# Kernel tuning notes

Hardware: AMD Instinct MI355X
Metric: run time of the kernel (lower is better)

## Reference

```python
import jax, jax.numpy as jnp
import numpy as np

N, P, T, D = 25000, 100000, 4, 128
DIN = 4 * D + 4  # 516
LEAKY = 0.001


def setup_inputs() -> dict:
    key = jax.random.key(0)
    ks = jax.random.split(key, 12)
    inp = {
        "coords": jax.random.normal(ks[0], (N, T, 3), jnp.float32),
        "propers": jax.random.randint(ks[1], (P, 4), 0, N, jnp.int64),
        "encoded": jax.random.normal(ks[2], (N, D), jnp.float32),
        "t": jax.random.uniform(ks[3], (T,), jnp.float32),
        "answer": jax.random.normal(ks[4], (N, T, 3), jnp.float32),
        # AggregateMLP(516 -> 128 -> 128 -> 128 -> 2), LeakyReLU(0.001) between
        "W0": jax.random.normal(ks[5], (DIN, D), jnp.float32) / np.sqrt(DIN),
        "b0": jnp.zeros((D,), jnp.float32),
        "W1": jax.random.normal(ks[6], (D, D), jnp.float32) / np.sqrt(D),
        "b1": jnp.zeros((D,), jnp.float32),
        "W2": jax.random.normal(ks[7], (D, D), jnp.float32) / np.sqrt(D),
        "b2": jnp.zeros((D,), jnp.float32),
        "W3": jax.random.normal(ks[8], (D, 2), jnp.float32) / np.sqrt(D),
        "b3": jnp.zeros((2,), jnp.float32),
    }
    return inp


def _forward(coords, propers, encoded, t, answer, W0, b0, W1, b1, W2, b2, W3, b3):
    p0, p1, p2, p3 = propers[:, 0], propers[:, 1], propers[:, 2], propers[:, 3]
    c0, c1, c2, c3 = coords[p0], coords[p1], coords[p2], coords[p3]  # [P,T,3]
    u1 = c1 - c0
    u2 = c2 - c1
    u3 = c3 - c2
    u1xu2 = jnp.cross(u1, u2, axis=-1)
    u2xu3 = jnp.cross(u2, u3, axis=-1)
    u2_norm = jnp.linalg.norm(u2, axis=-1, keepdims=True)
    u1yu2 = u1 * u2_norm
    theta = jnp.arctan2((u1yu2 * u2xu3).sum(-1), (u1xu2 * u2xu3).sum(-1))  # [P,T]
    dr = c0 - c3  # [P,T,3]
    dl = jnp.sqrt(jnp.clip(jnp.square(dr).sum(-1), 1e-12))  # [P,T]
    dh = dr / dl[..., None]

    Pn, Tn = propers.shape[0], t.shape[0]
    bcast = lambda e: jnp.broadcast_to(e[:, None, :], (Pn, Tn, e.shape[-1]))
    feats = jnp.concatenate(
        [
            bcast(encoded[p0]),
            bcast(encoded[p1]),
            bcast(encoded[p2]),
            bcast(encoded[p3]),
            jnp.broadcast_to(t.reshape(1, Tn, 1), (Pn, Tn, 1)),
            jnp.sin(theta)[..., None],
            jnp.cos(theta)[..., None],
            dl[..., None],
        ],
        axis=2,
    )  # [P,T,516]

    h = jax.nn.leaky_relu(feats @ W0 + b0, LEAKY)
    h = jax.nn.leaky_relu(h @ W1 + b1, LEAKY)
    h = jax.nn.leaky_relu(h @ W2 + b2, LEAKY)
    delta = h @ W3 + b3  # [P,T,2]

    out = answer.at[p0].add(-0.5 * delta[:, :, 0:1] * dh)
    out = out.at[p3].add(0.5 * delta[:, :, 1:2] * dh)
    return out


def reference(coords, propers, encoded, t, answer, W0, b0, W1, b1, W2, b2, W3, b3):
    return _forward(coords, propers, encoded, t, answer, W0, b0, W1, b1, W2, b2, W3, b3)
```

## Files before the change

### kernel.cpp

```cpp
#include <hip/hip_runtime.h>
#include <hip/hip_bf16.h>

#define NN 25000
#define PP 100000
#define TT 4
#define DD 128
#define LEAKY 0.001f

#define PB 32
#define ROWS 128

typedef __bf16 bf16;
typedef __bf16 bf16x8 __attribute__((ext_vector_type(8)));
typedef float  f32x4  __attribute__((ext_vector_type(4)));

#define OFF_W0SW  0u
#define OFF_W1SW  131072u
#define OFF_W2SW  163840u
#define OFF_W3SW  196608u
#define OFF_WTB   200704u
#define OFF_W5B   201728u
#define OFF_E     202496u
#define WS_END    25802496u

#define PR_W0SW  65536
#define PR_W1SW  16384
#define PR_W2SW  16384
#define PR_W3SW  2048
#define PR_WTB   512
#define PR_W5B   384
#define PR_COPY4 75000
#define PR_TOTAL (PR_W0SW + PR_W1SW + PR_W2SW + PR_W3SW + PR_WTB + PR_W5B + PR_COPY4)

__global__ __launch_bounds__(256) void prep_kernel(
    const float* __restrict__ W0, const float* __restrict__ W1,
    const float* __restrict__ W2, const float* __restrict__ W3,
    const float* __restrict__ answer, const float* __restrict__ tvec,
    const float* __restrict__ b0,
    bf16* __restrict__ W0sw, bf16* __restrict__ W1sw, bf16* __restrict__ W2sw,
    bf16* __restrict__ W3sw, bf16* __restrict__ WtB, bf16* __restrict__ W5B,
    float* __restrict__ out)
{
    int idx = blockIdx.x * 256 + threadIdx.x;
    if (idx < PR_W0SW) {
        int j = idx & 7, lane = (idx >> 3) & 63, c = idx >> 9;
        int fr = lane & 15, quad = lane >> 4;
        int kc = c & 15, iwv = c >> 4;
        int k = kc * 32 + quad * 8 + j;
        W0sw[idx] = (bf16)W0[k * 128 + iwv * 16 + fr];
        return;
    }
    idx -= PR_W0SW;
    if (idx < PR_W1SW) {
        int j = idx & 7, lane = (idx >> 3) & 63, c = idx >> 9;
        int fr = lane & 15, quad = lane >> 4;
        int kc = c & 3, nt = c >> 2;
        int k = kc * 32 + quad * 8 + j;
        W1sw[idx] = (bf16)W1[k * 128 + nt * 16 + fr];
        return;
    }
    idx -= PR_W1SW;
    if (idx < PR_W2SW) {
        int j = idx & 7, lane = (idx >> 3) & 63, c = idx >> 9;
        int fr = lane & 15, quad = lane >> 4;
        int kc = c & 3, nt = c >> 2;
        int k = kc * 32 + quad * 8 + j;
        W2sw[idx] = (bf16)W2[k * 128 + nt * 16 + fr];
        return;
    }
    idx -= PR_W2SW;
    if (idx < PR_W3SW) {
        int j = idx & 7, lane = (idx >> 3) & 63, kc = idx >> 9;
        int fr = lane & 15, quad = lane >> 4;
        int k = kc * 32 + quad * 8 + j;
        W3sw[idx] = (fr < 2) ? (bf16)W3[k * 2 + fr] : (bf16)0.0f;
        return;
    }
    idx -= PR_W3SW;
    if (idx < PR_WTB) {
        int t = idx >> 7, j = idx & 127;
        WtB[idx] = (bf16)(tvec[t] * W0[512 * 128 + j] + b0[j]);
        return;
    }
    idx -= PR_WTB;
    if (idx < PR_W5B) {
        W5B[idx] = (bf16)W0[(513 + (idx >> 7)) * 128 + (idx & 127)];
        return;
    }
    idx -= PR_W5B;
    if (idx < PR_COPY4) { ((float4*)out)[idx] = ((const float4*)answer)[idx]; }
}

__global__ __launch_bounds__(512) void prep_e_kernel(
    const float* __restrict__ encoded, const bf16* __restrict__ W0sw,
    bf16* __restrict__ E)
{
    __shared__ bf16 sA[128][136];
    __shared__ bf16 sT[128][40];
    const int tid = threadIdx.x;
    const int row0 = (blockIdx.x >> 2) * 128;
    const int ntb  = blockIdx.x & 3;
    for (int c = tid; c < 4096; c += 512) {
        int row = c >> 5, seg = c & 31;
        int rr = row0 + row; if (rr >= NN) rr = NN - 1;
        float4 v = *(const float4*)(encoded + (size_t)rr * 128 + seg * 4);
        bf16 pk[4] = {(bf16)v.x, (bf16)v.y, (bf16)v.z, (bf16)v.w};
        *(uint2*)(&sA[row][seg * 4]) = *(const uint2*)pk;
    }
    __syncthreads();
    const int wv = tid >> 6, lane = tid & 63;
    const int fr = lane & 15, quad = lane >> 4;
    const bf16* aBase = &sA[wv * 16 + fr][quad * 8];
    bf16x8 aFv[4];
    #pragma unroll
    for (int kcc = 0; kcc < 4; ++kcc) aFv[kcc] = *(const bf16x8*)(aBase + kcc * 32);
    const int orow = tid >> 2, oseg = tid & 3;
    #pragma unroll
    for (int i = 0; i < 4; ++i) {
        #pragma unroll
        for (int ntl = 0; ntl < 2; ++ntl) {
            int nt = ntb * 2 + ntl;
            f32x4 acc = {0.f, 0.f, 0.f, 0.f};
            #pragma unroll
            for (int kcc = 0; kcc < 4; ++kcc) {
                bf16x8 bF = *(const bf16x8*)(W0sw + ((size_t)nt * 16 + i * 4 + kcc) * 512 + lane * 8);
                acc = __builtin_amdgcn_mfma_f32_16x16x32_bf16(aFv[kcc], bF, acc, 0, 0, 0);
            }
            #pragma unroll
            for (int reg = 0; reg < 4; ++reg)
                sT[wv * 16 + quad * 4 + reg][ntl * 16 + fr] = (bf16)acc[reg];
        }
        __syncthreads();
        if (row0 + orow < NN)
            *(bf16x8*)(E + ((size_t)i * NN + row0 + orow) * 128 + ntb * 32 + oseg * 8) =
                *(const bf16x8*)(&sT[orow][oseg * 8]);
        __syncthreads();
    }
}

__global__ __launch_bounds__(512, 4) void main_kernel(
    const float* __restrict__ coords, const int* __restrict__ propers,
    const float* __restrict__ b1, const float* __restrict__ b2,
    const float* __restrict__ b3,
    const bf16* __restrict__ E, const bf16* __restrict__ W1sw,
    const bf16* __restrict__ W2sw, const bf16* __restrict__ W3sw,
    const bf16* __restrict__ WtB, const bf16* __restrict__ W5B,
    float* __restrict__ out)
{
    __shared__ bf16 sBuf0[ROWS * 136];
    __shared__ bf16 sBuf1[ROWS * 136];
    #define SH0(r, j) sBuf0[(r) * 136 + (j)]
    #define SH1(r, j) sBuf1[(r) * 136 + (j)]
    __shared__ int   sNodes[PB][4];
    __shared__ float sSn[ROWS], sCs[ROWS], sDl[ROWS], sDh[ROWS][3];
    __shared__ float sDelta[ROWS][2];

    const int tid  = threadIdx.x;
    const int pBase = blockIdx.x * PB;
    const int wv = tid >> 6, lane = tid & 63;
    const int fr = lane & 15, quad = lane >> 4;
    const int m2 = (wv & 3) * 2;
    const int nh = wv >> 2;

    const int p  = tid >> 4, s8 = tid & 15;
    bf16x8 e0, e1, e2, e3;
    {
        int4 pv = *(const int4*)(propers + (pBase + p) * 4);
        if (s8 == 0) { sNodes[p][0] = pv.x; sNodes[p][1] = pv.y;
                       sNodes[p][2] = pv.z; sNodes[p][3] = pv.w; }
        e0 = *(const bf16x8*)(E + ((size_t)0 * NN + pv.x) * 128 + s8 * 8);
        e1 = *(const bf16x8*)(E + ((size_t)1 * NN + pv.y) * 128 + s8 * 8);
        e2 = *(const bf16x8*)(E + ((size_t)2 * NN + pv.z) * 128 + s8 * 8);
        e3 = *(const bf16x8*)(E + ((size_t)3 * NN + pv.w) * 128 + s8 * 8);
    }
    bf16x8 w1f[16];
    {
        const bf16* w1b = W1sw + lane * 8;
        #pragma unroll
        for (int nt = 0; nt < 4; ++nt)
            #pragma unroll
            for (int kc = 0; kc < 4; ++kc)
                w1f[nt * 4 + kc] = *(const bf16x8*)(w1b + ((nh * 4 + nt) * 4 + kc) * 512);
    }
    if (tid < ROWS) {
        int r = tid, pp = r >> 2, t = r & 3;
        int4 pv = *(const int4*)(propers + (pBase + pp) * 4);
        const float* c0 = coords + pv.x * 12 + t * 3;
        const float* c1 = coords + pv.y * 12 + t * 3;
        const float* c2 = coords + pv.z * 12 + t * 3;
        const float* c3 = coords + pv.w * 12 + t * 3;
        float u1x = c1[0]-c0[0], u1y = c1[1]-c0[1], u1z = c1[2]-c0[2];
        float u2x = c2[0]-c1[0], u2y = c2[1]-c1[1], u2z = c2[2]-c1[2];
        float u3x = c3[0]-c2[0], u3y = c3[1]-c2[1], u3z = c3[2]-c2[2];
        float ax = u1y*u2z - u1z*u2y, ay = u1z*u2x - u1x*u2z, az = u1x*u2y - u1y*u2x;
        float bx = u2y*u3z - u2z*u3y, by = u2z*u3x - u2x*u3z, bz = u2x*u3y - u2y*u3x;
        float u2n = sqrtf(u2x*u2x + u2y*u2y + u2z*u2z);
        float num = u2n * (u1x*bx + u1y*by + u1z*bz);
        float den = ax*bx + ay*by + az*bz;
        float hyp = sqrtf(num*num + den*den);
        float sn, cs;
        if (hyp > 1e-30f) { float ih = 1.0f / hyp; sn = num * ih; cs = den * ih; }
        else { sn = 0.0f; cs = 1.0f; }
        float drx = c0[0]-c3[0], dry = c0[1]-c3[1], drz = c0[2]-c3[2];
        float dl = sqrtf(fmaxf(drx*drx + dry*dry + drz*drz, 1e-12f));
        float il = 1.0f / dl;
        sSn[r] = sn; sCs[r] = cs; sDl[r] = dl;
        sDh[r][0] = drx * il; sDh[r][1] = dry * il; sDh[r][2] = drz * il;
    }
    __syncthreads();

    {
        float g[8], w3f[8], w4f[8], w5f[8];
        #pragma unroll
        for (int j = 0; j < 8; ++j)
            g[j] = (float)e0[j] + (float)e1[j] + (float)e2[j] + (float)e3[j];
        bf16x8 w3v = *(const bf16x8*)(W5B + 0 * 128 + s8 * 8);
        bf16x8 w4v = *(const bf16x8*)(W5B + 1 * 128 + s8 * 8);
        bf16x8 w5v = *(const bf16x8*)(W5B + 2 * 128 + s8 * 8);
        #pragma unroll
        for (int j = 0; j < 8; ++j) {
            w3f[j] = (float)w3v[j]; w4f[j] = (float)w4v[j]; w5f[j] = (float)w5v[j];
        }
        #pragma unroll
        for (int t = 0; t < 4; ++t) {
            int r = p * 4 + t;
            bf16x8 wtv = *(const bf16x8*)(WtB + t * 128 + s8 * 8);
            float sn = sSn[r], cs = sCs[r], dl = sDl[r];
            bf16 hv[8];
            #pragma unroll
            for (int j = 0; j < 8; ++j) {
                float v = g[j] + (float)wtv[j] + sn * w3f[j] + cs * w4f[j] + dl * w5f[j];
                v = fmaxf(v, LEAKY * v);
                hv[j] = (bf16)v;
            }
            *(bf16x8*)(&SH0(r, s8 * 8)) = *(const bf16x8*)hv;
        }
    }
    __syncthreads();

    #pragma unroll
    for (int s = 0; s < 2; ++s) {
        f32x4 hacc[4];
        #pragma unroll
        for (int nt = 0; nt < 4; ++nt) hacc[nt] = (f32x4){0.f,0.f,0.f,0.f};
        const bf16* aRow = &SH0((m2 + s) * 16 + fr, quad * 8);
        #pragma unroll
        for (int kc = 0; kc < 4; ++kc) {
            bf16x8 aF = *(const bf16x8*)(aRow + kc * 32);
            #pragma unroll
            for (int nt = 0; nt < 4; ++nt)
                hacc[nt] = __builtin_amdgcn_mfma_f32_16x16x32_bf16(aF, w1f[nt * 4 + kc], hacc[nt], 0, 0, 0);
        }
        #pragma unroll
        for (int nt = 0; nt < 4; ++nt) {
            int j = (nh * 4 + nt) * 16 + fr;
            float bb = b1[j];
            #pragma unroll
            for (int reg = 0; reg < 4; ++reg) {
                int r = (m2 + s) * 16 + quad * 4 + reg;
                float v = hacc[nt][reg] + bb;
                v = fmaxf(v, LEAKY * v);
                SH1(r, j) = (bf16)v;
            }
        }
    }
    __syncthreads();

    #pragma unroll
    for (int s = 0; s < 2; ++s) {
        f32x4 hacc[4];
        #pragma unroll
        for (int nt = 0; nt < 4; ++nt) hacc[nt] = (f32x4){0.f,0.f,0.f,0.f};
        const bf16* aRow = &SH1((m2 + s) * 16 + fr, quad * 8);
        const bf16* w2b = W2sw + lane * 8;
        #pragma unroll
        for (int kc = 0; kc < 4; ++kc) {
            bf16x8 aF = *(const bf16x8*)(aRow + kc * 32);
            #pragma unroll
            for (int nt = 0; nt < 4; ++nt) {
                bf16x8 bF = *(const bf16x8*)(w2b + ((nh * 4 + nt) * 4 + kc) * 512);
                hacc[nt] = __builtin_amdgcn_mfma_f32_16x16x32_bf16(aF, bF, hacc[nt], 0, 0, 0);
            }
        }
        #pragma unroll
        for (int nt = 0; nt < 4; ++nt) {
            int j = (nh * 4 + nt) * 16 + fr;
            float bb = b2[j];
            #pragma unroll
            for (int reg = 0; reg < 4; ++reg) {
                int r = (m2 + s) * 16 + quad * 4 + reg;
                float v = hacc[nt][reg] + bb;
                v = fmaxf(v, LEAKY * v);
                SH0(r, j) = (bf16)v;
            }
        }
    }
    __syncthreads();

    {
        f32x4 dacc = {0.f,0.f,0.f,0.f};
        const bf16* aRow = &SH0(wv * 16 + fr, quad * 8);
        const bf16* w3b = W3sw + lane * 8;
        #pragma unroll
        for (int kc = 0; kc < 4; ++kc) {
            bf16x8 aF = *(const bf16x8*)(aRow + kc * 32);
            bf16x8 bF = *(const bf16x8*)(w3b + kc * 512);
            dacc = __builtin_amdgcn_mfma_f32_16x16x32_bf16(aF, bF, dacc, 0, 0, 0);
        }
        if (fr < 2) {
            float bb = b3[fr];
            #pragma unroll
            for (int reg = 0; reg < 4; ++reg)
                sDelta[wv * 16 + quad * 4 + reg][fr] = dacc[reg] + bb;
        }
    }
    __syncthreads();

    for (int idx = tid; idx < ROWS * 6; idx += 512) {
        int r = idx / 6, c = idx % 6;
        int pp = r >> 2, t = r & 3;
        int side = c / 3, ax = c % 3;
        int node = sNodes[pp][side ? 3 : 0];
        float dval = side ? 0.5f * sDelta[r][1] : -0.5f * sDelta[r][0];
        atomicAdd(out + node * 12 + t * 3 + ax, dval * sDh[r][ax]);
    }
    #undef SH0
    #undef SH1
}

extern "C" void kernel_launch(void* const* d_in, const int* in_sizes, int n_in,
                              void* d_out, int out_size, void* d_ws, size_t ws_size,
                              hipStream_t stream) {
    const float* coords  = (const float*)d_in[0];
    const int*   propers = (const int*)d_in[1];
    const float* encoded = (const float*)d_in[2];
    const float* tvec    = (const float*)d_in[3];
    const float* answer  = (const float*)d_in[4];
    const float* W0 = (const float*)d_in[5];
    const float* b0 = (const float*)d_in[6];
    const float* W1 = (const float*)d_in[7];
    const float* b1 = (const float*)d_in[8];
    const float* W2 = (const float*)d_in[9];
    const float* b2 = (const float*)d_in[10];
    const float* W3 = (const float*)d_in[11];
    const float* b3 = (const float*)d_in[12];
    float* out = (float*)d_out;
    char* ws = (char*)d_ws;
    bf16* W0sw = (bf16*)(ws + OFF_W0SW);
    bf16* W1sw = (bf16*)(ws + OFF_W1SW);
    bf16* W2sw = (bf16*)(ws + OFF_W2SW);
    bf16* W3sw = (bf16*)(ws + OFF_W3SW);
    bf16* WtB  = (bf16*)(ws + OFF_WTB);
    bf16* W5B  = (bf16*)(ws + OFF_W5B);
    bf16* E    = (bf16*)(ws + OFF_E);

    int prep_blocks = (PR_TOTAL + 255) / 256;
    prep_kernel<<<prep_blocks, 256, 0, stream>>>(W0, W1, W2, W3, answer, tvec, b0,
                                                 W0sw, W1sw, W2sw, W3sw, WtB, W5B, out);
    prep_e_kernel<<<196 * 4, 512, 0, stream>>>(encoded, W0sw, E);
    main_kernel<<<PP / PB, 512, 0, stream>>>(coords, propers, b1, b2, b3,
                                             E, W1sw, W2sw, W3sw, WtB, W5B, out);
}
```

Before: 195.7 us.

## Make each wave own its own 16-row tile and drop block-wide barriers

Restructures the main kernel so each of the 8 waves independently processes 4 propers (16 rows) end to end, with a per-wave shared-memory tile reused across layers. This replaces the __syncthreads barriers with wave-local lgkmcnt waits. Geometry values now travel by lane shuffles instead of shared arrays. W1 is no longer held in registers, so each wave computes all 128 output columns and streams W1/W2 fragments from global memory. Launch bounds rise to 6 blocks per CU to allow more occupancy, at the cost of more weight reloads per wave and a tighter register budget.

```diff
diff --git a/kernel.cpp b/kernel.cpp
--- a/kernel.cpp
+++ b/kernel.cpp
@@ -138,7 +138,7 @@
     }
 }
 
-__global__ __launch_bounds__(512, 4) void main_kernel(
+__global__ __launch_bounds__(512, 6) void main_kernel(
     const float* __restrict__ coords, const int* __restrict__ propers,
     const float* __restrict__ b1, const float* __restrict__ b2,
     const float* __restrict__ b3,
@@ -147,48 +147,35 @@
     const bf16* __restrict__ WtB, const bf16* __restrict__ W5B,
     float* __restrict__ out)
 {
-    __shared__ bf16 sBuf0[ROWS * 136];
-    __shared__ bf16 sBuf1[ROWS * 136];
-    #define SH0(r, j) sBuf0[(r) * 136 + (j)]
-    #define SH1(r, j) sBuf1[(r) * 136 + (j)]
-    __shared__ int   sNodes[PB][4];
-    __shared__ float sSn[ROWS], sCs[ROWS], sDl[ROWS], sDh[ROWS][3];
-    __shared__ float sDelta[ROWS][2];
+    __shared__ __align__(16) bf16 sH[8][16][136];
+    __shared__ float sScr[8][16][6];
+    __shared__ int   sNd[8][8];
 
     const int tid  = threadIdx.x;
-    const int pBase = blockIdx.x * PB;
-    const int wv = tid >> 6, lane = tid & 63;
-    const int fr = lane & 15, quad = lane >> 4;
-    const int m2 = (wv & 3) * 2;
-    const int nh = wv >> 2;
-
-    const int p  = tid >> 4, s8 = tid & 15;
-    bf16x8 e0, e1, e2, e3;
-    {
-        int4 pv = *(const int4*)(propers + (pBase + p) * 4);
-        if (s8 == 0) { sNodes[p][0] = pv.x; sNodes[p][1] = pv.y;
-                       sNodes[p][2] = pv.z; sNodes[p][3] = pv.w; }
-        e0 = *(const bf16x8*)(E + ((size_t)0 * NN + pv.x) * 128 + s8 * 8);
-        e1 = *(const bf16x8*)(E + ((size_t)1 * NN + pv.y) * 128 + s8 * 8);
-        e2 = *(const bf16x8*)(E + ((size_t)2 * NN + pv.z) * 128 + s8 * 8);
-        e3 = *(const bf16x8*)(E + ((size_t)3 * NN + pv.w) * 128 + s8 * 8);
-    }
-    bf16x8 w1f[16];
-    {
-        const bf16* w1b = W1sw + lane * 8;
-        #pragma unroll
-        for (int nt = 0; nt < 4; ++nt)
-            #pragma unroll
-            for (int kc = 0; kc < 4; ++kc)
-                w1f[nt * 4 + kc] = *(const bf16x8*)(w1b + ((nh * 4 + nt) * 4 + kc) * 512);
-    }
-    if (tid < ROWS) {
-        int r = tid, pp = r >> 2, t = r & 3;
-        int4 pv = *(const int4*)(propers + (pBase + pp) * 4);
-        const float* c0 = coords + pv.x * 12 + t * 3;
-        const float* c1 = coords + pv.y * 12 + t * 3;
-        const float* c2 = coords + pv.z * 12 + t * 3;
-        const float* c3 = coords + pv.w * 12 + t * 3;
+    const int wv   = tid >> 6, lane = tid & 63;
+    const int fr   = lane & 15, quad = lane >> 4;
+    const int pw   = blockIdx.x * PB + wv * 4;
+
+#define LGKM0() asm volatile("s_waitcnt lgkmcnt(0)" ::: "memory")
+
+    int4 pv = *(const int4*)(propers + (size_t)(pw + quad) * 4);
+    bf16x8 e0 = *(const bf16x8*)(E + ((size_t)0 * NN + pv.x) * 128 + fr * 8);
+    bf16x8 e1 = *(const bf16x8*)(E + ((size_t)1 * NN + pv.y) * 128 + fr * 8);
+    bf16x8 e2 = *(const bf16x8*)(E + ((size_t)2 * NN + pv.z) * 128 + fr * 8);
+    bf16x8 e3 = *(const bf16x8*)(E + ((size_t)3 * NN + pv.w) * 128 + fr * 8);
+    if (fr == 0) { sNd[wv][quad * 2] = pv.x; sNd[wv][quad * 2 + 1] = pv.w; }
+    bf16x8 w3v = *(const bf16x8*)(W5B + 0 * 128 + fr * 8);
+    bf16x8 w4v = *(const bf16x8*)(W5B + 1 * 128 + fr * 8);
+    bf16x8 w5v = *(const bf16x8*)(W5B + 2 * 128 + fr * 8);
+
+    float snl = 0.f, csl = 1.f, dll = 0.f;
+    if (lane < 16) {
+        int pp_ = lane >> 2, t = lane & 3;
+        int4 pg = *(const int4*)(propers + (size_t)(pw + pp_) * 4);
+        const float* c0 = coords + (size_t)pg.x * 12 + t * 3;
+        const float* c1 = coords + (size_t)pg.y * 12 + t * 3;
+        const float* c2 = coords + (size_t)pg.z * 12 + t * 3;
+        const float* c3 = coords + (size_t)pg.w * 12 + t * 3;
         float u1x = c1[0]-c0[0], u1y = c1[1]-c0[1], u1z = c1[2]-c0[2];
         float u2x = c2[0]-c1[0], u2y = c2[1]-c1[1], u2z = c2[2]-c1[2];
         float u3x = c3[0]-c2[0], u3y = c3[1]-c2[1], u3z = c3[2]-c2[2];
@@ -198,34 +185,28 @@
         float num = u2n * (u1x*bx + u1y*by + u1z*bz);
         float den = ax*bx + ay*by + az*bz;
         float hyp = sqrtf(num*num + den*den);
-        float sn, cs;
-        if (hyp > 1e-30f) { float ih = 1.0f / hyp; sn = num * ih; cs = den * ih; }
-        else { sn = 0.0f; cs = 1.0f; }
+        if (hyp > 1e-30f) { float ih = 1.0f / hyp; snl = num * ih; csl = den * ih; }
+        else { snl = 0.0f; csl = 1.0f; }
         float drx = c0[0]-c3[0], dry = c0[1]-c3[1], drz = c0[2]-c3[2];
-        float dl = sqrtf(fmaxf(drx*drx + dry*dry + drz*drz, 1e-12f));
-        float il = 1.0f / dl;
-        sSn[r] = sn; sCs[r] = cs; sDl[r] = dl;
-        sDh[r][0] = drx * il; sDh[r][1] = dry * il; sDh[r][2] = drz * il;
-    }
-    __syncthreads();
+        dll = sqrtf(fmaxf(drx*drx + dry*dry + drz*drz, 1e-12f));
+        float il = 1.0f / dll;
+        sScr[wv][lane][0] = drx * il;
+        sScr[wv][lane][1] = dry * il;
+        sScr[wv][lane][2] = drz * il;
+    }
 
     {
         float g[8], w3f[8], w4f[8], w5f[8];
         #pragma unroll
-        for (int j = 0; j < 8; ++j)
-            g[j] = (float)e0[j] + (float)e1[j] + (float)e2[j] + (float)e3[j];
-        bf16x8 w3v = *(const bf16x8*)(W5B + 0 * 128 + s8 * 8);
-        bf16x8 w4v = *(const bf16x8*)(W5B + 1 * 128 + s8 * 8);
-        bf16x8 w5v = *(const bf16x8*)(W5B + 2 * 128 + s8 * 8);
-        #pragma unroll
         for (int j = 0; j < 8; ++j) {
+            g[j]   = (float)e0[j] + (float)e1[j] + (float)e2[j] + (float)e3[j];
             w3f[j] = (float)w3v[j]; w4f[j] = (float)w4v[j]; w5f[j] = (float)w5v[j];
         }
         #pragma unroll
         for (int t = 0; t < 4; ++t) {
-            int r = p * 4 + t;
-            bf16x8 wtv = *(const bf16x8*)(WtB + t * 128 + s8 * 8);
-            float sn = sSn[r], cs = sCs[r], dl = sDl[r];
+            int r = quad * 4 + t;
+            bf16x8 wtv = *(const bf16x8*)(WtB + t * 128 + fr * 8);
+            float sn = __shfl(snl, r), cs = __shfl(csl, r), dl = __shfl(dll, r);
             bf16 hv[8];
             #pragma unroll
             for (int j = 0; j < 8; ++j) {
@@ -233,99 +214,82 @@
                 v = fmaxf(v, LEAKY * v);
                 hv[j] = (bf16)v;
             }
-            *(bf16x8*)(&SH0(r, s8 * 8)) = *(const bf16x8*)hv;
-        }
-    }
-    __syncthreads();
-
-    #pragma unroll
-    for (int s = 0; s < 2; ++s) {
-        f32x4 hacc[4];
-        #pragma unroll
-        for (int nt = 0; nt < 4; ++nt) hacc[nt] = (f32x4){0.f,0.f,0.f,0.f};
-        const bf16* aRow = &SH0((m2 + s) * 16 + fr, quad * 8);
+            *(bf16x8*)(&sH[wv][r][fr * 8]) = *(const bf16x8*)hv;
+        }
+    }
+
+#define DENSE_LAYER(Wsw, bvec)                                                  \
+    {                                                                           \
+        LGKM0();        \
+        bf16x8 aF[4];                                                           \
+        const bf16* aRow = &sH[wv][fr][quad * 8];                               \
+        _Pragma("unroll")                                                       \
+        for (int kc = 0; kc < 4; ++kc)                                          \
+            aF[kc] = *(const bf16x8*)(aRow + kc * 32);                          \
+        LGKM0();      \
+        _Pragma("unroll")                                                       \
+        for (int hh = 0; hh < 2; ++hh) {                                        \
+            f32x4 acc[4];                                                       \
+            _Pragma("unroll")                                                   \
+            for (int nt = 0; nt < 4; ++nt) acc[nt] = (f32x4){0.f,0.f,0.f,0.f};  \
+            _Pragma("unroll")                                                   \
+            for (int kc = 0; kc < 4; ++kc) {                                    \
+                _Pragma("unroll")                                               \
+                for (int nt = 0; nt < 4; ++nt) {                                \
+                    bf16x8 bF = *(const bf16x8*)(Wsw +                          \
+                        ((size_t)((hh * 4 + nt) * 4 + kc)) * 512 + lane * 8);   \
+                    acc[nt] = __builtin_amdgcn_mfma_f32_16x16x32_bf16(          \
+                        aF[kc], bF, acc[nt], 0, 0, 0);                          \
+                }                                                               \
+            }                                                                   \
+            _Pragma("unroll")                                                   \
+            for (int nt = 0; nt < 4; ++nt) {                                    \
+                int j = (hh * 4 + nt) * 16 + fr;                                \
+                float bb = bvec[j];                                             \
+                _Pragma("unroll")                                               \
+                for (int reg = 0; reg < 4; ++reg) {                             \
+                    float v = acc[nt][reg] + bb;                                \
+                    v = fmaxf(v, LEAKY * v);                                    \
+                    sH[wv][quad * 4 + reg][j] = (bf16)v;                        \
+                }                                                               \
+            }                                                                   \
+        }                                                                       \
+    }
+
+    DENSE_LAYER(W1sw, b1)
+    DENSE_LAYER(W2sw, b2)
+
+    {
+        LGKM0();
+        bf16x8 aF[4];
+        const bf16* aRow = &sH[wv][fr][quad * 8];
+        #pragma unroll
+        for (int kc = 0; kc < 4; ++kc)
+            aF[kc] = *(const bf16x8*)(aRow + kc * 32);
+        f32x4 dacc = {0.f, 0.f, 0.f, 0.f};
         #pragma unroll
         for (int kc = 0; kc < 4; ++kc) {
-            bf16x8 aF = *(const bf16x8*)(aRow + kc * 32);
-            #pragma unroll
-            for (int nt = 0; nt < 4; ++nt)
-                hacc[nt] = __builtin_amdgcn_mfma_f32_16x16x32_bf16(aF, w1f[nt * 4 + kc], hacc[nt], 0, 0, 0);
-        }
-        #pragma unroll
-        for (int nt = 0; nt < 4; ++nt) {
-            int j = (nh * 4 + nt) * 16 + fr;
-            float bb = b1[j];
-            #pragma unroll
-            for (int reg = 0; reg < 4; ++reg) {
-                int r = (m2 + s) * 16 + quad * 4 + reg;
-                float v = hacc[nt][reg] + bb;
-                v = fmaxf(v, LEAKY * v);
-                SH1(r, j) = (bf16)v;
-            }
-        }
-    }
-    __syncthreads();
-
-    #pragma unroll
-    for (int s = 0; s < 2; ++s) {
-        f32x4 hacc[4];
-        #pragma unroll
-        for (int nt = 0; nt < 4; ++nt) hacc[nt] = (f32x4){0.f,0.f,0.f,0.f};
-        const bf16* aRow = &SH1((m2 + s) * 16 + fr, quad * 8);
-        const bf16* w2b = W2sw + lane * 8;
-        #pragma unroll
-        for (int kc = 0; kc < 4; ++kc) {
-            bf16x8 aF = *(const bf16x8*)(aRow + kc * 32);
-            #pragma unroll
-            for (int nt = 0; nt < 4; ++nt) {
-                bf16x8 bF = *(const bf16x8*)(w2b + ((nh * 4 + nt) * 4 + kc) * 512);
-                hacc[nt] = __builtin_amdgcn_mfma_f32_16x16x32_bf16(aF, bF, hacc[nt], 0, 0, 0);
-            }
-        }
-        #pragma unroll
-        for (int nt = 0; nt < 4; ++nt) {
-            int j = (nh * 4 + nt) * 16 + fr;
-            float bb = b2[j];
-            #pragma unroll
-            for (int reg = 0; reg < 4; ++reg) {
-                int r = (m2 + s) * 16 + quad * 4 + reg;
-                float v = hacc[nt][reg] + bb;
-                v = fmaxf(v, LEAKY * v);
-                SH0(r, j) = (bf16)v;
-            }
-        }
-    }
-    __syncthreads();
-
-    {
-        f32x4 dacc = {0.f,0.f,0.f,0.f};
-        const bf16* aRow = &SH0(wv * 16 + fr, quad * 8);
-        const bf16* w3b = W3sw + lane * 8;
-        #pragma unroll
-        for (int kc = 0; kc < 4; ++kc) {
-            bf16x8 aF = *(const bf16x8*)(aRow + kc * 32);
-            bf16x8 bF = *(const bf16x8*)(w3b + kc * 512);
-            dacc = __builtin_amdgcn_mfma_f32_16x16x32_bf16(aF, bF, dacc, 0, 0, 0);
+            bf16x8 bF = *(const bf16x8*)(W3sw + (size_t)kc * 512 + lane * 8);
+            dacc = __builtin_amdgcn_mfma_f32_16x16x32_bf16(aF[kc], bF, dacc, 0, 0, 0);
         }
         if (fr < 2) {
             float bb = b3[fr];
             #pragma unroll
             for (int reg = 0; reg < 4; ++reg)
-                sDelta[wv * 16 + quad * 4 + reg][fr] = dacc[reg] + bb;
-        }
-    }
-    __syncthreads();
-
-    for (int idx = tid; idx < ROWS * 6; idx += 512) {
-        int r = idx / 6, c = idx % 6;
-        int pp = r >> 2, t = r & 3;
-        int side = c / 3, ax = c % 3;
-        int node = sNodes[pp][side ? 3 : 0];
-        float dval = side ? 0.5f * sDelta[r][1] : -0.5f * sDelta[r][0];
-        atomicAdd(out + node * 12 + t * 3 + ax, dval * sDh[r][ax]);
-    }
-    #undef SH0
-    #undef SH1
+                sScr[wv][quad * 4 + reg][3 + fr] = dacc[reg] + bb;
+        }
+    }
+
+    LGKM0();
+    for (int idx = lane; idx < 96; idx += 64) {
+        int r = idx / 6, c = idx - (idx / 6) * 6;
+        int side = c / 3, ax = c - side * 3;
+        int node = sNd[wv][(r >> 2) * 2 + side];
+        float dval = (side ? 0.5f : -0.5f) * sScr[wv][r][3 + side];
+        atomicAdd(out + (size_t)node * 12 + (r & 3) * 3 + ax, dval * sScr[wv][r][ax]);
+    }
+#undef DENSE_LAYER
+#undef LGKM0
 }
 
 extern "C" void kernel_launch(void* const* d_in, const int* in_sizes, int n_in,
```

Measured after the change: 202.6 us. 3.5% more time.
